# Performance work log

Hardware: AMD Instinct MI355X
Metric: run time of the kernel (lower is better)

## Reference

```python
import jax, jax.numpy as jnp
import numpy as np

N_NODES = 100000
N_EDGES = 1600000
IN_CH = 256
OUT_CH = 32
HEADS = 4
NEG_SLOPE = 0.2


def setup_inputs() -> dict:
    key = jax.random.key(0)
    k1, k2, k3, k4, k5 = jax.random.split(key, 5)
    x = jax.random.normal(k1, (N_NODES, IN_CH), dtype=jnp.float32)
    edge_index = jax.random.randint(k2, (2, N_EDGES), 0, N_NODES, dtype=jnp.int64)
    hc = HEADS * OUT_CH
    # glorot init like the torch module
    std_w = np.sqrt(6.0 / (hc + IN_CH))
    W = jax.random.uniform(k3, (hc, IN_CH), dtype=jnp.float32, minval=-std_w, maxval=std_w)
    b = jnp.zeros((hc,), dtype=jnp.float32)
    std_a = np.sqrt(6.0 / (hc + 2))
    att = jax.random.uniform(k4, (hc, 2), dtype=jnp.float32, minval=-std_a, maxval=std_a)
    return {"x": x, "edge_index": edge_index, "W": W, "b": b, "att": att}


def reference(x, edge_index, W, b, att):
    # flow = 'target_to_source': tid=0, sid=1
    tar = edge_index[0]
    src = edge_index[1]
    feat = x @ W.T + b                      # [N, H*C]
    e_pre = feat @ att                      # [N, 2]
    e_src = e_pre[:, 0:1]                   # [N, 1]
    e_tar = e_pre[:, 1:2]                   # [N, 1]
    # edge scores
    e = jnp.exp(jax.nn.leaky_relu(e_src[src] + e_tar[tar], negative_slope=NEG_SLOPE))   # [E, 1]
    e_self = jnp.exp(jax.nn.leaky_relu(e_src + e_tar, negative_slope=NEG_SLOPE))        # [N, 1]
    # softmax denominator over incoming edges + self loop
    e_sum = jax.ops.segment_sum(e, tar, num_segments=N_NODES) + e_self                  # [N, 1]
    alpha_self = e_self / e_sum             # [N, 1]
    alpha = e / e_sum[tar]                  # [E, 1]
    # weighted aggregation (dropout=0 / eval -> identity)
    out = jax.ops.segment_sum(feat[src] * alpha, tar, num_segments=N_NODES)
    out = out + feat * alpha_self           # [N, H*C], concat=True
    return out
```

## Files before the change

### kernel.cpp

```cpp
#include <hip/hip_runtime.h>
#include <hip/hip_bf16.h>
#include <math.h>

#define N_NODES 100000
#define N_EDGES 1600000
#define IN_CH 256
#define HC 128
#define NEG_SLOPE 0.2f

#define NB_C 196
#define CCAP 8704
#define CHUNK 3200

#define GBM 128
#define GEMM_BLOCKS 782
#define BIN_BLOCKS 500

typedef __attribute__((ext_vector_type(8))) short short8;
typedef __attribute__((ext_vector_type(4))) float floatx4;

__device__ inline ushort f2b(float f) {
    __hip_bfloat16 h = __float2bfloat16(f);
    return *(ushort*)&h;
}

__device__ inline float edge_e(float z) {
    float lr = z > 0.f ? z : NEG_SLOPE * z;
    return __expf(lr);
}

__device__ inline float bflo(unsigned u) { return __uint_as_float(u << 16); }
__device__ inline float bfhi(unsigned u) { return __uint_as_float(u & 0xffff0000u); }

__global__ __launch_bounds__(256, 2)
void fused_gemm_bin_k(const float* __restrict__ x, const float* __restrict__ W,
                      const float* __restrict__ b, const float* __restrict__ att,
                      __hip_bfloat16* __restrict__ featb,
                      float* __restrict__ e_src, float* __restrict__ e_tar,
                      float* __restrict__ e_self,
                      const int* __restrict__ ei, int* __restrict__ gcur,
                      int* __restrict__ ebuf) {
    __shared__ ushort xs[128][72];
    __shared__ ushort wsh[128][72];
    __shared__ int lcnt[NB_C];
    __shared__ int lcur[NB_C];

    const int tid = threadIdx.x;

    if (blockIdx.x >= GEMM_BLOCKS) {
        const int base = (blockIdx.x - GEMM_BLOCKS) * CHUNK;

        for (int i = tid; i < NB_C; i += 256) lcnt[i] = 0;
        __syncthreads();

        for (int i = tid; i < CHUNK; i += 256)
            atomicAdd(&lcnt[ei[base + i] >> 9], 1);
        __syncthreads();

        for (int bkt = tid; bkt < NB_C; bkt += 256) {
            int c = lcnt[bkt];
            lcur[bkt] = c ? atomicAdd(&gcur[bkt], c) : 0;
        }
        __syncthreads();

        for (int i = tid; i < CHUNK; i += 256) {
            int t = ei[base + i];
            int s = ei[N_EDGES + base + i];
            int bkt = t >> 9;
            int pos = atomicAdd(&lcur[bkt], 1);
            if (pos < CCAP)
                ebuf[bkt * CCAP + pos] = s | ((t & 511) << 17);
        }
        return;
    }

    const int wave = tid >> 6;
    const int lane = tid & 63;
    const int l16  = lane >> 4;
    const int lc   = lane & 15;
    const int row0 = blockIdx.x * GBM;

    floatx4 acc[2][8];
    #pragma unroll
    for (int mt = 0; mt < 2; ++mt)
        #pragma unroll
        for (int nt = 0; nt < 8; ++nt)
            acc[mt][nt] = (floatx4){0.f, 0.f, 0.f, 0.f};

    const int r  = tid >> 4;
    const int kq = tid & 15;

    for (int kb = 0; kb < 4; ++kb) {
        float4 xv[8];
        #pragma unroll
        for (int i = 0; i < 8; ++i) {
            int gr = row0 + r + i * 16;
            int grc = gr < N_NODES ? gr : N_NODES - 1;
            xv[i] = *(const float4*)&x[(size_t)grc * IN_CH + kb * 64 + kq * 4];
        }
        float4 wv[8];
        #pragma unroll
        for (int i = 0; i < 8; ++i)
            wv[i] = *(const float4*)&W[(size_t)(r + i * 16) * IN_CH + kb * 64 + kq * 4];

        #pragma unroll
        for (int i = 0; i < 8; ++i) {
            ushort4 u;
            u.x = f2b(xv[i].x); u.y = f2b(xv[i].y);
            u.z = f2b(xv[i].z); u.w = f2b(xv[i].w);
            *(ushort4*)&xs[r + i * 16][kq * 4] = u;
        }
        #pragma unroll
        for (int i = 0; i < 8; ++i) {
            ushort4 u;
            u.x = f2b(wv[i].x); u.y = f2b(wv[i].y);
            u.z = f2b(wv[i].z); u.w = f2b(wv[i].w);
            *(ushort4*)&wsh[r + i * 16][kq * 4] = u;
        }

        __syncthreads();
        #pragma unroll
        for (int ks = 0; ks < 2; ++ks) {
            short8 a0 = *(short8*)&xs[wave * 32 + lc][ks * 32 + l16 * 8];
            short8 a1 = *(short8*)&xs[wave * 32 + 16 + lc][ks * 32 + l16 * 8];
            short8 bf[8];
            #pragma unroll
            for (int nt = 0; nt < 8; ++nt)
                bf[nt] = *(short8*)&wsh[nt * 16 + lc][ks * 32 + l16 * 8];
            #pragma unroll
            for (int nt = 0; nt < 8; ++nt) {
                acc[0][nt] = __builtin_amdgcn_mfma_f32_16x16x32_bf16(a0, bf[nt], acc[0][nt], 0, 0, 0);
                acc[1][nt] = __builtin_amdgcn_mfma_f32_16x16x32_bf16(a1, bf[nt], acc[1][nt], 0, 0, 0);
            }
        }
        __syncthreads();
    }

    float av0[8], av1[8], bc[8];
    #pragma unroll
    for (int nt = 0; nt < 8; ++nt) {
        float2 av = *(const float2*)&att[(nt * 16 + lc) * 2];
        av0[nt] = av.x; av1[nt] = av.y;
        bc[nt] = b[nt * 16 + lc];
    }

    #pragma unroll
    for (int mt = 0; mt < 2; ++mt) {
        #pragma unroll
        for (int rg = 0; rg < 4; ++rg) {
            int row = row0 + wave * 32 + mt * 16 + l16 * 4 + rg;
            float s = 0.f, t = 0.f;
            float vals[8];
            #pragma unroll
            for (int nt = 0; nt < 8; ++nt) {
                float v = acc[mt][nt][rg] + bc[nt];
                vals[nt] = v;
                s += v * av0[nt];
                t += v * av1[nt];
            }
            #pragma unroll
            for (int off = 8; off; off >>= 1) {
                s += __shfl_xor(s, off);
                t += __shfl_xor(t, off);
            }
            if (row < N_NODES) {
                if (lc == 0) {
                    e_src[row] = s;
                    e_tar[row] = t;
                    float z = s + t;
                    float lr = z > 0.f ? z : NEG_SLOPE * z;
                    e_self[row] = __expf(lr);
                }
                #pragma unroll
                for (int nt = 0; nt < 8; ++nt)
                    featb[(size_t)row * HC + nt * 16 + lc] = __float2bfloat16(vals[nt]);
            }
        }
    }
}

__global__ __launch_bounds__(512)
void bucket_csr2_k(const int* __restrict__ gcur, const int* __restrict__ ebuf,
                   const float* __restrict__ e_src, const float* __restrict__ e_tar,
                   int* __restrict__ offsets, int* __restrict__ csr_src,
                   float* __restrict__ ewb) {
    const int b = blockIdx.x;
    const int tid = threadIdx.x;
    const int lane = tid & 63;

    __shared__ int sc[256];
    __shared__ int lcnt[512];
    __shared__ int wsum[8];
    __shared__ int lout[CCAP];
    __shared__ float ltar[512];

    {
        int n = b * 512 + tid;
        ltar[tid] = (n < N_NODES) ? e_tar[n] : 0.f;
    }

    if (tid < 256) {
        int c = 0;
        if (tid < NB_C) { c = gcur[tid]; if (c > CCAP) c = CCAP; }
        sc[tid] = c;
    }
    lcnt[tid] = 0;
    __syncthreads();
    #pragma unroll
    for (int off = 1; off < 256; off <<= 1) {
        int v = 0;
        if (tid < 256) v = sc[tid] + ((tid >= off) ? sc[tid - off] : 0);
        __syncthreads();
        if (tid < 256) sc[tid] = v;
        __syncthreads();
    }
    int count = gcur[b]; if (count > CCAP) count = CCAP;
    const int base = (b == 0) ? 0 : sc[b - 1];

    const int* st = &ebuf[b * CCAP];
    for (int i = tid; i < count; i += 512)
        atomicAdd(&lcnt[st[i] >> 17], 1);
    __syncthreads();

    int cnt = lcnt[tid];
    int v = cnt;
    #pragma unroll
    for (int off = 1; off < 64; off <<= 1) {
        int t = __shfl_up(v, off);
        if (lane >= off) v += t;
    }
    if (lane == 63) wsum[tid >> 6] = v;
    __syncthreads();
    if (tid < 64) {
        int w = (tid < 8) ? wsum[tid] : 0;
        #pragma unroll
        for (int off = 1; off < 8; off <<= 1) {
            int t = __shfl_up(w, off);
            if (lane >= off) w += t;
        }
        if (tid < 8) wsum[tid] = w;
    }
    __syncthreads();
    int wbase = (tid >= 64) ? wsum[(tid >> 6) - 1] : 0;
    int excl = v + wbase - cnt;
    __syncthreads();
    lcnt[tid] = excl;

    {
        int n0 = b * 512 + tid;
        if (n0 < N_NODES) offsets[n0] = base + excl;
    }
    if (b == NB_C - 1 && tid == 0) offsets[N_NODES] = base + count;
    __syncthreads();

    for (int i = tid; i < count; i += 512) {
        int v2 = st[i];
        int pos = atomicAdd(&lcnt[v2 >> 17], 1);
        lout[pos] = v2;
    }
    __syncthreads();

    for (int i = tid; i < count; i += 512) {
        int v2 = lout[i];
        int src = v2 & 0x1FFFF;
        csr_src[base + i] = src;
        ewb[base + i] = edge_e(e_src[src] + ltar[v2 >> 17]);
    }
}

__global__ __launch_bounds__(256)
void aggregate_k(const int* __restrict__ offsets, const int* __restrict__ csr_src,
                 const float* __restrict__ ewb,
                 const __hip_bfloat16* __restrict__ featb,
                 const float* __restrict__ e_self, float* __restrict__ out) {
    int node = blockIdx.x * 4 + (threadIdx.x >> 6);
    if (node >= N_NODES) return;
    int lane = threadIdx.x & 63;
    int g = lane >> 4;
    int q = lane & 15;
    int beg = offsets[node];
    int end = offsets[node + 1];
    float eself = e_self[node];

    const char* fb = (const char*)featb;
    const size_t qofs = (size_t)(q * 16);

    uint4 su = *(const uint4*)(fb + (size_t)node * 256 + qofs);
    float m0 = (g == 0) ? eself : 0.f;
    float esum = m0;
    float acc[8];
    acc[0] = m0 * bflo(su.x); acc[1] = m0 * bfhi(su.x);
    acc[2] = m0 * bflo(su.y); acc[3] = m0 * bfhi(su.y);
    acc[4] = m0 * bflo(su.z); acc[5] = m0 * bfhi(su.z);
    acc[6] = m0 * bflo(su.w); acc[7] = m0 * bfhi(su.w);

    int j = beg;
    for (; j + 7 < end; j += 8) {
        int s0 = csr_src[j + g];
        int s1 = csr_src[j + 4 + g];
        float e0 = ewb[j + g];
        float e1 = ewb[j + 4 + g];
        uint4 u0 = *(const uint4*)(fb + (size_t)s0 * 256 + qofs);
        uint4 u1 = *(const uint4*)(fb + (size_t)s1 * 256 + qofs);
        esum += e0 + e1;
        acc[0] += e0 * bflo(u0.x) + e1 * bflo(u1.x);
        acc[1] += e0 * bfhi(u0.x) + e1 * bfhi(u1.x);
        acc[2] += e0 * bflo(u0.y) + e1 * bflo(u1.y);
        acc[3] += e0 * bfhi(u0.y) + e1 * bfhi(u1.y);
        acc[4] += e0 * bflo(u0.z) + e1 * bflo(u1.z);
        acc[5] += e0 * bfhi(u0.z) + e1 * bfhi(u1.z);
        acc[6] += e0 * bflo(u0.w) + e1 * bflo(u1.w);
        acc[7] += e0 * bfhi(u0.w) + e1 * bfhi(u1.w);
    }
    for (; j + 3 < end; j += 4) {
        int s0 = csr_src[j + g];
        float e0 = ewb[j + g];
        uint4 u0 = *(const uint4*)(fb + (size_t)s0 * 256 + qofs);
        esum += e0;
        acc[0] += e0 * bflo(u0.x);
        acc[1] += e0 * bfhi(u0.x);
        acc[2] += e0 * bflo(u0.y);
        acc[3] += e0 * bfhi(u0.y);
        acc[4] += e0 * bflo(u0.z);
        acc[5] += e0 * bfhi(u0.z);
        acc[6] += e0 * bflo(u0.w);
        acc[7] += e0 * bfhi(u0.w);
    }
    for (; j < end; ++j) {
        int s0 = csr_src[j];
        float ew = ewb[j];
        uint4 u0 = *(const uint4*)(fb + (size_t)s0 * 256 + qofs);
        float em = (g == 0) ? ew : 0.f;
        esum += em;
        acc[0] += em * bflo(u0.x);
        acc[1] += em * bfhi(u0.x);
        acc[2] += em * bflo(u0.y);
        acc[3] += em * bfhi(u0.y);
        acc[4] += em * bflo(u0.z);
        acc[5] += em * bfhi(u0.z);
        acc[6] += em * bflo(u0.w);
        acc[7] += em * bfhi(u0.w);
    }

    #pragma unroll
    for (int k = 0; k < 8; ++k) {
        acc[k] += __shfl_xor(acc[k], 16);
        acc[k] += __shfl_xor(acc[k], 32);
    }
    esum += __shfl_xor(esum, 16);
    esum += __shfl_xor(esum, 32);

    if (g == 0) {
        float inv = 1.f / esum;
        float* op = &out[(size_t)node * HC + q * 8];
        *(float4*)op = make_float4(acc[0] * inv, acc[1] * inv, acc[2] * inv, acc[3] * inv);
        *(float4*)(op + 4) = make_float4(acc[4] * inv, acc[5] * inv, acc[6] * inv, acc[7] * inv);
    }
}

extern "C" void kernel_launch(void* const* d_in, const int* in_sizes, int n_in,
                              void* d_out, int out_size, void* d_ws, size_t ws_size,
                              hipStream_t stream) {
    const float* x   = (const float*)d_in[0];
    const int*   ei  = (const int*)d_in[1];
    const float* W   = (const float*)d_in[2];
    const float* b   = (const float*)d_in[3];
    const float* att = (const float*)d_in[4];
    float* out = (float*)d_out;

    unsigned char* p = (unsigned char*)d_ws;
    auto take = [&](size_t bytes) {
        unsigned char* r = p;
        p += (bytes + 255) & ~(size_t)255;
        return (void*)r;
    };
    __hip_bfloat16* featb = (__hip_bfloat16*)take((size_t)N_NODES * HC * sizeof(__hip_bfloat16));
    float* e_src   = (float*)take((size_t)N_NODES * sizeof(float));
    float* e_tar   = (float*)take((size_t)N_NODES * sizeof(float));
    float* e_self  = (float*)take((size_t)N_NODES * sizeof(float));
    int*   offsets = (int*)take((size_t)(N_NODES + 1) * sizeof(int));
    int*   gcur    = (int*)take((size_t)NB_C * sizeof(int));
    int*   csr_src = (int*)take((size_t)N_EDGES * sizeof(int));
    float* ewb     = (float*)take((size_t)N_EDGES * sizeof(float));
    int*   ebuf    = (int*)take((size_t)NB_C * CCAP * sizeof(int));

    (void)hipMemsetAsync(gcur, 0, NB_C * sizeof(int), stream);

    fused_gemm_bin_k<<<GEMM_BLOCKS + BIN_BLOCKS, 256, 0, stream>>>(
        x, W, b, att, featb, e_src, e_tar, e_self, ei, gcur, ebuf);

    bucket_csr2_k<<<NB_C, 512, 0, stream>>>(gcur, ebuf, e_src, e_tar,
                                            offsets, csr_src, ewb);

    aggregate_k<<<(N_NODES + 3) / 4, 256, 0, stream>>>(offsets, csr_src, ewb,
                                                       featb, e_self, out);
}
```

Baseline: 292.8 us.

## Stage full W in LDS once and load x operands directly into registers

After: 299.7 us. 1.02x slower.

```diff
diff --git a/kernel.cpp b/kernel.cpp
--- a/kernel.cpp
+++ b/kernel.cpp
@@ -15,6 +15,7 @@
 #define GBM 128
 #define GEMM_BLOCKS 782
 #define BIN_BLOCKS 500
+#define WPAD 264
 
 typedef __attribute__((ext_vector_type(8))) short short8;
 typedef __attribute__((ext_vector_type(4))) float floatx4;
@@ -31,6 +32,10 @@
 
 __device__ inline float bflo(unsigned u) { return __uint_as_float(u << 16); }
 __device__ inline float bfhi(unsigned u) { return __uint_as_float(u & 0xffff0000u); }
+
+union U8 { short8 v; ushort u[8]; };
+
+extern __shared__ unsigned char smem[];
 
 __global__ __launch_bounds__(256, 2)
 void fused_gemm_bin_k(const float* __restrict__ x, const float* __restrict__ W,
@@ -40,14 +45,11 @@
                       float* __restrict__ e_self,
                       const int* __restrict__ ei, int* __restrict__ gcur,
                       int* __restrict__ ebuf) {
-    __shared__ ushort xs[128][72];
-    __shared__ ushort wsh[128][72];
-    __shared__ int lcnt[NB_C];
-    __shared__ int lcur[NB_C];
-
     const int tid = threadIdx.x;
 
     if (blockIdx.x >= GEMM_BLOCKS) {
+        int* lcnt = (int*)smem;
+        int* lcur = lcnt + NB_C;
         const int base = (blockIdx.x - GEMM_BLOCKS) * CHUNK;
 
         for (int i = tid; i < NB_C; i += 256) lcnt[i] = 0;
@@ -74,12 +76,33 @@
         return;
     }
 
+    ushort (*wsh)[WPAD] = (ushort (*)[WPAD])smem;
     const int wave = tid >> 6;
     const int lane = tid & 63;
     const int l16  = lane >> 4;
     const int lc   = lane & 15;
     const int row0 = blockIdx.x * GBM;
 
+    #pragma unroll 4
+    for (int i = 0; i < 32; ++i) {
+        int fidx = tid + i * 256;
+        float4 v = *(const float4*)&W[(size_t)fidx * 4];
+        ushort4 u;
+        u.x = f2b(v.x); u.y = f2b(v.y); u.z = f2b(v.z); u.w = f2b(v.w);
+        *(ushort4*)&wsh[fidx >> 6][(fidx & 63) * 4] = u;
+    }
+    __syncthreads();
+
+    int r0c, r1c;
+    {
+        int r0 = row0 + wave * 32 + lc;
+        int r1 = r0 + 16;
+        r0c = r0 < N_NODES ? r0 : N_NODES - 1;
+        r1c = r1 < N_NODES ? r1 : N_NODES - 1;
+    }
+    const float* xb0 = &x[(size_t)r0c * IN_CH + l16 * 8];
+    const float* xb1 = &x[(size_t)r1c * IN_CH + l16 * 8];
+
     floatx4 acc[2][8];
     #pragma unroll
     for (int mt = 0; mt < 2; ++mt)
@@ -87,54 +110,54 @@
         for (int nt = 0; nt < 8; ++nt)
             acc[mt][nt] = (floatx4){0.f, 0.f, 0.f, 0.f};
 
-    const int r  = tid >> 4;
-    const int kq = tid & 15;
-
-    for (int kb = 0; kb < 4; ++kb) {
-        float4 xv[8];
-        #pragma unroll
-        for (int i = 0; i < 8; ++i) {
-            int gr = row0 + r + i * 16;
-            int grc = gr < N_NODES ? gr : N_NODES - 1;
-            xv[i] = *(const float4*)&x[(size_t)grc * IN_CH + kb * 64 + kq * 4];
-        }
-        float4 wv[8];
-        #pragma unroll
-        for (int i = 0; i < 8; ++i)
-            wv[i] = *(const float4*)&W[(size_t)(r + i * 16) * IN_CH + kb * 64 + kq * 4];
-
-        #pragma unroll
-        for (int i = 0; i < 8; ++i) {
-            ushort4 u;
-            u.x = f2b(xv[i].x); u.y = f2b(xv[i].y);
-            u.z = f2b(xv[i].z); u.w = f2b(xv[i].w);
-            *(ushort4*)&xs[r + i * 16][kq * 4] = u;
-        }
-        #pragma unroll
-        for (int i = 0; i < 8; ++i) {
-            ushort4 u;
-            u.x = f2b(wv[i].x); u.y = f2b(wv[i].y);
-            u.z = f2b(wv[i].z); u.w = f2b(wv[i].w);
-            *(ushort4*)&wsh[r + i * 16][kq * 4] = u;
-        }
-
-        __syncthreads();
-        #pragma unroll
-        for (int ks = 0; ks < 2; ++ks) {
-            short8 a0 = *(short8*)&xs[wave * 32 + lc][ks * 32 + l16 * 8];
-            short8 a1 = *(short8*)&xs[wave * 32 + 16 + lc][ks * 32 + l16 * 8];
-            short8 bf[8];
-            #pragma unroll
-            for (int nt = 0; nt < 8; ++nt)
-                bf[nt] = *(short8*)&wsh[nt * 16 + lc][ks * 32 + l16 * 8];
-            #pragma unroll
-            for (int nt = 0; nt < 8; ++nt) {
-                acc[0][nt] = __builtin_amdgcn_mfma_f32_16x16x32_bf16(a0, bf[nt], acc[0][nt], 0, 0, 0);
-                acc[1][nt] = __builtin_amdgcn_mfma_f32_16x16x32_bf16(a1, bf[nt], acc[1][nt], 0, 0, 0);
-            }
-        }
-        __syncthreads();
-    }
+#define ISSUE(dst, kb) do { \
+    dst[0][0][0] = *(const float4*)(xb0 + (kb) * 64); \
+    dst[0][0][1] = *(const float4*)(xb0 + (kb) * 64 + 4); \
+    dst[0][1][0] = *(const float4*)(xb0 + (kb) * 64 + 32); \
+    dst[0][1][1] = *(const float4*)(xb0 + (kb) * 64 + 36); \
+    dst[1][0][0] = *(const float4*)(xb1 + (kb) * 64); \
+    dst[1][0][1] = *(const float4*)(xb1 + (kb) * 64 + 4); \
+    dst[1][1][0] = *(const float4*)(xb1 + (kb) * 64 + 32); \
+    dst[1][1][1] = *(const float4*)(xb1 + (kb) * 64 + 36); \
+} while (0)
+
+#define CVT(d, pa, pb) do { \
+    d.u[0] = f2b(pa.x); d.u[1] = f2b(pa.y); d.u[2] = f2b(pa.z); d.u[3] = f2b(pa.w); \
+    d.u[4] = f2b(pb.x); d.u[5] = f2b(pb.y); d.u[6] = f2b(pb.z); d.u[7] = f2b(pb.w); \
+} while (0)
+
+#define PROC(src, kb) do { \
+    U8 a00, a01, a10, a11; \
+    CVT(a00, src[0][0][0], src[0][0][1]); \
+    CVT(a01, src[0][1][0], src[0][1][1]); \
+    CVT(a10, src[1][0][0], src[1][0][1]); \
+    CVT(a11, src[1][1][0], src[1][1][1]); \
+    _Pragma("unroll") \
+    for (int ks = 0; ks < 2; ++ks) { \
+        short8 aa0 = ks ? a01.v : a00.v; \
+        short8 aa1 = ks ? a11.v : a10.v; \
+        _Pragma("unroll") \
+        for (int nt = 0; nt < 8; ++nt) { \
+            short8 bf = *(short8*)&wsh[nt * 16 + lc][(kb) * 64 + ks * 32 + l16 * 8]; \
+            acc[0][nt] = __builtin_amdgcn_mfma_f32_16x16x32_bf16(aa0, bf, acc[0][nt], 0, 0, 0); \
+            acc[1][nt] = __builtin_amdgcn_mfma_f32_16x16x32_bf16(aa1, bf, acc[1][nt], 0, 0, 0); \
+        } \
+    } \
+} while (0)
+
+    float4 v0[2][2][2], v1[2][2][2], v2[2][2][2], v3[2][2][2];
+    ISSUE(v0, 0);
+    ISSUE(v1, 1);
+    PROC(v0, 0);
+    ISSUE(v2, 2);
+    ISSUE(v3, 3);
+    PROC(v1, 1);
+    PROC(v2, 2);
+    PROC(v3, 3);
+
+#undef ISSUE
+#undef CVT
+#undef PROC
 
     float av0[8], av1[8], bc[8];
     #pragma unroll
@@ -386,7 +409,7 @@
 
     (void)hipMemsetAsync(gcur, 0, NB_C * sizeof(int), stream);
 
-    fused_gemm_bin_k<<<GEMM_BLOCKS + BIN_BLOCKS, 256, 0, stream>>>(
+    fused_gemm_bin_k<<<GEMM_BLOCKS + BIN_BLOCKS, 256, 128 * WPAD * 2, stream>>>(
         x, W, b, att, featb, e_src, e_tar, e_self, ei, gcur, ebuf);
 
     bucket_csr2_k<<<NB_C, 512, 0, stream>>>(gcur, ebuf, e_src, e_tar,
```
